# Kernel tuning notes

Hardware: AMD Instinct MI355X
Metric: run time of the kernel (lower is better)

The kernel has to match this reference:

```python
import jax, jax.numpy as jnp
import numpy as np
import math

RCR = 5.2
NUM_SPECIES = 4
TARGET_SIZE = 1008
ETA_R = jnp.asarray([16.0], dtype=jnp.float32)  # (1,)
SHF_R = jnp.asarray([0.9, 1.16875, 1.4375, 1.70625, 1.975, 2.24375, 2.5125, 2.78125,
                     3.05, 3.31875, 3.5875, 3.85625, 4.125, 4.39375, 4.6625, 4.93125],
                    dtype=jnp.float32)  # (16,)


def setup_inputs() -> dict:
    key = jax.random.key(0)
    k1, k2 = jax.random.split(key)
    B, N = 4, 1024
    species = jax.random.randint(k1, (B, N), 0, NUM_SPECIES, dtype=jnp.int64)
    coordinates = jax.random.normal(k2, (B, N, 3), dtype=jnp.float32)
    return {"species": species, "coordinates": coordinates}


def reference(species, coordinates):
    B, N = species.shape
    # pairwise differences and distances (safe sqrt so the i==j diagonal is exact 0)
    diff = coordinates[:, :, None, :] - coordinates[:, None, :, :]  # (B,N,N,3)
    d2 = jnp.sum(diff * diff, axis=-1)                               # (B,N,N)
    nonzero = d2 > 0
    dist = jnp.sqrt(jnp.where(nonzero, d2, 1.0)) * nonzero           # (B,N,N)
    mask = (dist > 0) & (dist <= RCR)
    # cosine cutoff
    fc = (0.5 * jnp.cos(math.pi * dist / RCR) + 0.5) * mask.astype(dist.dtype)  # (B,N,N)
    # per-species one-hot of neighbor atoms
    onehot = jax.nn.one_hot(species, NUM_SPECIES, dtype=dist.dtype)  # (B,N,S)
    # Gaussian radial shells: (B,N,N,K) with K = len(ShfR) (EtaR broadcasts)
    core = jnp.exp(-ETA_R[None, None, None, :] * 0.0 - ETA_R * (dist[..., None] - SHF_R) ** 2)
    core = jnp.exp(-ETA_R * (dist[..., None] - SHF_R) ** 2)          # (B,N,N,K)
    # radial[b,i,s,k] = sum_j core[b,i,j,k] * fc[b,i,j] * onehot[b,j,s]
    radial = jnp.einsum('bijk,bij,bjs->bisk', core, fc, onehot)      # (B,N,S,K)
    radial_vec = radial.reshape(B, N, NUM_SPECIES * SHF_R.shape[0])  # s outer, k inner (matches torch cat)
    pad = TARGET_SIZE - radial_vec.shape[-1]
    if pad > 0:
        radial_vec = jnp.concatenate(
            [radial_vec, jnp.zeros((B, N, pad), dtype=radial_vec.dtype)], axis=-1)
    return radial_vec
```

## Files before the change

### kernel.cpp

```cpp
#include <hip/hip_runtime.h>

#define NATOMS 1024
#define NBATCH 4
#define TSIZE  1008

typedef float v2f __attribute__((ext_vector_type(2)));

__global__ __launch_bounds__(512, 6) void aev_fused_kernel(
    const int* __restrict__ species,
    const float* __restrict__ coords,
    float* __restrict__ out)
{
    __shared__ float2 lxy[NATOMS];
    __shared__ float  lz[NATOMS];
    __shared__ int    cnt[16][4];
    __shared__ int    basearr[16][4];
    __shared__ int    lseg[5];

    const int tid      = threadIdx.x;
    const int b        = blockIdx.x >> 8;
    const int atomBase = (blockIdx.x & 255) * 4;
    const int lane     = tid & 63;
    const int w        = tid >> 6;

    const unsigned long long lt = (1ull << lane) - 1ull;

    int sp_[2], rank_[2];
#pragma unroll
    for (int c = 0; c < 2; ++c) {
        const int g  = 8 * c + w;
        const int a  = 64 * g + lane;
        const int sp = species[b * NATOMS + a];
        sp_[c] = sp;
        int r = 0;
#pragma unroll
        for (int s = 0; s < 4; ++s) {
            const unsigned long long m = __ballot(sp == s);
            if (sp == s) r = __popcll(m & lt);
            if (lane == 0) cnt[g][s] = __popcll(m);
        }
        rank_[c] = r;
    }
    __syncthreads();

    if (w == 0) {
        const int s = lane >> 4, g = lane & 15;
        const int v = cnt[g][s];
        int inc = v;
#pragma unroll
        for (int off = 1; off < 64; off <<= 1) {
            const int u = __shfl_up(inc, off, 64);
            if (lane >= off) inc += u;
        }
        const int exc = inc - v;
        basearr[g][s] = exc;
        if (g == 0)     lseg[s] = exc;
        if (lane == 63) lseg[4] = inc;
    }
    __syncthreads();

#pragma unroll
    for (int c = 0; c < 2; ++c) {
        const int g   = 8 * c + w;
        const int a   = 64 * g + lane;
        const int pos = basearr[g][sp_[c]] + rank_[c];
        const float x = coords[(b * NATOMS + a) * 3 + 0];
        const float y = coords[(b * NATOMS + a) * 3 + 1];
        const float z = coords[(b * NATOMS + a) * 3 + 2];
        lxy[pos] = make_float2(x, y);
        lz[pos]  = z;
    }

    {
        const float4 z4 = make_float4(0.f, 0.f, 0.f, 0.f);
        for (int t = tid; t < 4 * 236; t += 512) {
            const int r = t / 236;
            const int c = t - r * 236;
            float4* p = reinterpret_cast<float4*>(
                out + (size_t)(b * NATOMS + atomBase + r) * TSIZE + 64 + c * 4);
            *p = z4;
        }
    }
    __syncthreads();

    const int aid = w >> 1;
    const int h   = w & 1;
    const int i   = atomBase + aid;
    const float cx = coords[(b * NATOMS + i) * 3 + 0];
    const float cy = coords[(b * NATOMS + i) * 3 + 1];
    const float cz = coords[(b * NATOMS + i) * 3 + 2];

    v2f accp[2][8];
#pragma unroll
    for (int sl = 0; sl < 2; ++sl)
#pragma unroll
        for (int m = 0; m < 8; ++m) accp[sl][m] = (v2f){0.f, 0.f};

#pragma unroll
    for (int sl = 0; sl < 2; ++sl) {
        const int s   = 2 * h + sl;
        const int beg = lseg[s];
        const int end = lseg[s + 1];
        for (int jj = beg + lane; jj < end; jj += 64) {
            const float2 xy = lxy[jj];
            const float  zz = lz[jj];
            const float dx = xy.x - cx;
            const float dy = xy.y - cy;
            const float dz = zz   - cz;
            const float d2 = fmaf(dx, dx, fmaf(dy, dy, dz * dz));
            const float d  = __builtin_amdgcn_sqrtf(d2);
            const float dc = fminf(d, 5.2f);
            const float fc = fmaf(0.5f, __builtin_amdgcn_cosf(dc * 0.09615384615f), 0.5f);

            const float t7 = fmaf(dc, 4.80448963f, -13.36248679f);
            const float a  = 2.5824132f * t7;
            float ed = __builtin_amdgcn_exp2f(-(t7 * t7));
            const float g  = __builtin_amdgcn_exp2f(a);
            const float gi = __builtin_amdgcn_exp2f(-a);
            ed *= fc;

            v2f e;
            e.x = ed;
            e.y = ed * (g * 0.3148664f);
            v2f r = (v2f){gi, g} * (v2f){0.3148664f, 0.0312141f};

            accp[sl][0] += e;
#pragma unroll
            for (int m = 1; m <= 7; ++m) {
                e *= r;
                r *= 0.0991402f;
                accp[sl][m] += e;
            }
        }
    }

    float acc[32];
#pragma unroll
    for (int sl = 0; sl < 2; ++sl) {
        acc[sl * 16 + 7] = accp[sl][0].x;
        acc[sl * 16 + 8] = accp[sl][0].y;
#pragma unroll
        for (int m = 1; m <= 7; ++m) {
            acc[sl * 16 + 7 - m] = accp[sl][m].x;
            acc[sl * 16 + 8 + m] = accp[sl][m].y;
        }
    }

#pragma unroll
    for (int q = 0; q < 16; ++q) {
        asm("v_permlane32_swap_b32 %0, %1" : "+v"(acc[q]), "+v"(acc[q + 16]));
        acc[q] += acc[q + 16];
    }
#pragma unroll
    for (int q = 0; q < 8; ++q) {
        asm("v_permlane16_swap_b32 %0, %1" : "+v"(acc[q]), "+v"(acc[q + 8]));
        acc[q] += acc[q + 8];
    }
#pragma unroll
    for (int step = 0; step < 3; ++step) {
        const int m = 8 >> step;
        const int n = 4 >> step;
        const bool hi = (lane & m) != 0;
#pragma unroll
        for (int q = 0; q < n; ++q) {
            const float keep = hi ? acc[q + n] : acc[q];
            const float send = hi ? acc[q] : acc[q + n];
            acc[q] = keep + __shfl_xor(send, m, 64);
        }
    }
    const float tot = acc[0] + __shfl_xor(acc[0], 1, 64);

    if (!(lane & 1))
        out[(size_t)(b * NATOMS + i) * TSIZE + h * 32 + (lane >> 1)] = tot;
}

extern "C" void kernel_launch(void* const* d_in, const int* in_sizes, int n_in,
                              void* d_out, int out_size, void* d_ws, size_t ws_size,
                              hipStream_t stream)
{
    const int*   species = (const int*)d_in[0];
    const float* coords  = (const float*)d_in[1];
    float* out = (float*)d_out;

    aev_fused_kernel<<<1024, 512, 0, stream>>>(species, coords, out);
}
```

Baseline: 18.65 us.

## Assign one wave per species segment and halve atoms per block

Each block now handles 2 atoms instead of 4, with one wave per (atom, species) pair, and the grid doubles to 2048 blocks. The per-wave accumulator state shrinks from two species slices to one. The loop software-prefetches the next neighbour's coordinates from LDS, and the zero-padding stores move after the compute loop. The cost is that every block repeats the species sort and LDS staging of all 1024 atoms, so twice as much of that setup work is done overall.

After: 29.47 us. +58.0%, slower.

```diff
diff --git a/kernel.cpp b/kernel.cpp
--- a/kernel.cpp
+++ b/kernel.cpp
@@ -6,7 +6,7 @@
 
 typedef float v2f __attribute__((ext_vector_type(2)));
 
-__global__ __launch_bounds__(512, 6) void aev_fused_kernel(
+__global__ __launch_bounds__(512, 8) void aev_fused_kernel(
     const int* __restrict__ species,
     const float* __restrict__ coords,
     float* __restrict__ out)
@@ -18,8 +18,8 @@
     __shared__ int    lseg[5];
 
     const int tid      = threadIdx.x;
-    const int b        = blockIdx.x >> 8;
-    const int atomBase = (blockIdx.x & 255) * 4;
+    const int b        = blockIdx.x >> 9;
+    const int atomBase = (blockIdx.x & 511) * 2;
     const int lane     = tid & 63;
     const int w        = tid >> 6;
 
@@ -70,87 +70,80 @@
         lxy[pos] = make_float2(x, y);
         lz[pos]  = z;
     }
-
-    {
-        const float4 z4 = make_float4(0.f, 0.f, 0.f, 0.f);
-        for (int t = tid; t < 4 * 236; t += 512) {
-            const int r = t / 236;
-            const int c = t - r * 236;
-            float4* p = reinterpret_cast<float4*>(
-                out + (size_t)(b * NATOMS + atomBase + r) * TSIZE + 64 + c * 4);
-            *p = z4;
-        }
-    }
     __syncthreads();
 
-    const int aid = w >> 1;
-    const int h   = w & 1;
+    const int aid = w >> 2;
+    const int s   = w & 3;
     const int i   = atomBase + aid;
     const float cx = coords[(b * NATOMS + i) * 3 + 0];
     const float cy = coords[(b * NATOMS + i) * 3 + 1];
     const float cz = coords[(b * NATOMS + i) * 3 + 2];
 
-    v2f accp[2][8];
+    v2f accp[8];
 #pragma unroll
-    for (int sl = 0; sl < 2; ++sl)
+    for (int m = 0; m < 8; ++m) accp[m] = (v2f){0.f, 0.f};
+
+    const int beg = lseg[s];
+    const int end = lseg[s + 1];
+
+    int jj = beg + lane;
+    float2 xy = lxy[jj & (NATOMS - 1)];
+    float  zz = lz[jj & (NATOMS - 1)];
+
+    while (jj < end) {
+        const int   jn  = jj + 64;
+        const int   jc  = jn & (NATOMS - 1);
+        const float2 xyn = lxy[jc];
+        const float  zn  = lz[jc];
+
+        const float dx = xy.x - cx;
+        const float dy = xy.y - cy;
+        const float dz = zz   - cz;
+        const float d2 = fmaf(dx, dx, fmaf(dy, dy, dz * dz));
+        const float d  = __builtin_amdgcn_sqrtf(d2);
+        const float dc = fminf(d, 5.2f);
+        const float fc = fmaf(0.5f, __builtin_amdgcn_cosf(dc * 0.09615384615f), 0.5f);
+
+        const float t7 = fmaf(dc, 4.80448963f, -13.36248679f);
+        const float a  = 2.5824132f * t7;
+        float ed = __builtin_amdgcn_exp2f(-(t7 * t7));
+        const float g  = __builtin_amdgcn_exp2f(a);
+        const float gi = __builtin_amdgcn_exp2f(-a);
+        ed *= fc;
+
+        v2f e;
+        e.x = ed;
+        e.y = ed * (g * 0.3148664f);
+        v2f r = (v2f){gi, g} * (v2f){0.3148664f, 0.0312141f};
+
+        accp[0] += e;
 #pragma unroll
-        for (int m = 0; m < 8; ++m) accp[sl][m] = (v2f){0.f, 0.f};
+        for (int m = 1; m <= 7; ++m) {
+            e *= r;
+            r *= 0.0991402f;
+            accp[m] += e;
+        }
 
-#pragma unroll
-    for (int sl = 0; sl < 2; ++sl) {
-        const int s   = 2 * h + sl;
-        const int beg = lseg[s];
-        const int end = lseg[s + 1];
-        for (int jj = beg + lane; jj < end; jj += 64) {
-            const float2 xy = lxy[jj];
-            const float  zz = lz[jj];
-            const float dx = xy.x - cx;
-            const float dy = xy.y - cy;
-            const float dz = zz   - cz;
-            const float d2 = fmaf(dx, dx, fmaf(dy, dy, dz * dz));
-            const float d  = __builtin_amdgcn_sqrtf(d2);
-            const float dc = fminf(d, 5.2f);
-            const float fc = fmaf(0.5f, __builtin_amdgcn_cosf(dc * 0.09615384615f), 0.5f);
-
-            const float t7 = fmaf(dc, 4.80448963f, -13.36248679f);
-            const float a  = 2.5824132f * t7;
-            float ed = __builtin_amdgcn_exp2f(-(t7 * t7));
-            const float g  = __builtin_amdgcn_exp2f(a);
-            const float gi = __builtin_amdgcn_exp2f(-a);
-            ed *= fc;
-
-            v2f e;
-            e.x = ed;
-            e.y = ed * (g * 0.3148664f);
-            v2f r = (v2f){gi, g} * (v2f){0.3148664f, 0.0312141f};
-
-            accp[sl][0] += e;
-#pragma unroll
-            for (int m = 1; m <= 7; ++m) {
-                e *= r;
-                r *= 0.0991402f;
-                accp[sl][m] += e;
-            }
-        }
+        jj = jn; xy = xyn; zz = zn;
     }
 
-    float acc[32];
-#pragma unroll
-    for (int sl = 0; sl < 2; ++sl) {
-        acc[sl * 16 + 7] = accp[sl][0].x;
-        acc[sl * 16 + 8] = accp[sl][0].y;
-#pragma unroll
-        for (int m = 1; m <= 7; ++m) {
-            acc[sl * 16 + 7 - m] = accp[sl][m].x;
-            acc[sl * 16 + 8 + m] = accp[sl][m].y;
-        }
+    if (tid < 2 * 236) {
+        const int r2 = tid / 236;
+        const int c2 = tid - r2 * 236;
+        float4* p = reinterpret_cast<float4*>(
+            out + (size_t)(b * NATOMS + atomBase + r2) * TSIZE + 64 + c2 * 4);
+        *p = make_float4(0.f, 0.f, 0.f, 0.f);
     }
 
+    float acc[16];
+    acc[7] = accp[0].x;
+    acc[8] = accp[0].y;
 #pragma unroll
-    for (int q = 0; q < 16; ++q) {
-        asm("v_permlane32_swap_b32 %0, %1" : "+v"(acc[q]), "+v"(acc[q + 16]));
-        acc[q] += acc[q + 16];
+    for (int m = 1; m <= 7; ++m) {
+        acc[7 - m] = accp[m].x;
+        acc[8 + m] = accp[m].y;
     }
+
 #pragma unroll
     for (int q = 0; q < 8; ++q) {
         asm("v_permlane16_swap_b32 %0, %1" : "+v"(acc[q]), "+v"(acc[q + 8]));
@@ -168,10 +161,11 @@
             acc[q] = keep + __shfl_xor(send, m, 64);
         }
     }
-    const float tot = acc[0] + __shfl_xor(acc[0], 1, 64);
+    float tot = acc[0] + __shfl_xor(acc[0], 1, 64);
+    tot += __shfl_xor(tot, 32, 64);
 
-    if (!(lane & 1))
-        out[(size_t)(b * NATOMS + i) * TSIZE + h * 32 + (lane >> 1)] = tot;
+    if (!(lane & 1) && lane < 32)
+        out[(size_t)(b * NATOMS + i) * TSIZE + s * 16 + (lane >> 1)] = tot;
 }
 
 extern "C" void kernel_launch(void* const* d_in, const int* in_sizes, int n_in,
@@ -182,5 +176,5 @@
     const float* coords  = (const float*)d_in[1];
     float* out = (float*)d_out;
 
-    aev_fused_kernel<<<1024, 512, 0, stream>>>(species, coords, out);
+    aev_fused_kernel<<<2048, 512, 0, stream>>>(species, coords, out);
 }
```
